# Performance work log

Measured on AMD Instinct MI355X. Metric: run time of the kernel, lower is better.

The kernel has to match this reference:

```python
import jax, jax.numpy as jnp
import numpy as np

B, S, H, L, V, T = 128, 512, 512, 2, 30, 64  # batch, enc len, hidden, layers, vocab, decode len


def _p(k, shape):
    return jax.random.normal(k, shape, jnp.float32) * 0.05


def setup_inputs() -> dict:
    key = jax.random.key(0)
    ks = jax.random.split(key, 24)
    inp = {"x": jax.random.normal(ks[0], (B, S, 2), jnp.float32)}
    inp["emb"] = _p(ks[1], (V, H))
    # encoder GRU (input dim 2 for layer 0, H for layer 1); PyTorch gate order r,z,n
    inp["enc_Wih0"] = _p(ks[2], (3 * H, 2));  inp["enc_Whh0"] = _p(ks[3], (3 * H, H))
    inp["enc_bih0"] = _p(ks[4], (3 * H,));    inp["enc_bhh0"] = _p(ks[5], (3 * H,))
    inp["enc_Wih1"] = _p(ks[6], (3 * H, H));  inp["enc_Whh1"] = _p(ks[7], (3 * H, H))
    inp["enc_bih1"] = _p(ks[8], (3 * H,));    inp["enc_bhh1"] = _p(ks[9], (3 * H,))
    # decoder GRU (input dim H)
    inp["dec_Wih0"] = _p(ks[10], (3 * H, H)); inp["dec_Whh0"] = _p(ks[11], (3 * H, H))
    inp["dec_bih0"] = _p(ks[12], (3 * H,));   inp["dec_bhh0"] = _p(ks[13], (3 * H,))
    inp["dec_Wih1"] = _p(ks[14], (3 * H, H)); inp["dec_Whh1"] = _p(ks[15], (3 * H, H))
    inp["dec_bih1"] = _p(ks[16], (3 * H,));   inp["dec_bhh1"] = _p(ks[17], (3 * H,))
    inp["fc_W"] = _p(ks[18], (V, 2 * H));     inp["fc_b"] = _p(ks[19], (V,))
    return inp


def gru_cell(xt, h, Wih, Whh, bih, bhh):
    gi = xt @ Wih.T + bih
    gh = h @ Whh.T + bhh
    i_r, i_z, i_n = jnp.split(gi, 3, axis=-1)
    h_r, h_z, h_n = jnp.split(gh, 3, axis=-1)
    r = jax.nn.sigmoid(i_r + h_r)
    z = jax.nn.sigmoid(i_z + h_z)
    n = jnp.tanh(i_n + r * h_n)
    return (1.0 - z) * n + z * h


def _forward(x, emb,
             enc_Wih0, enc_Whh0, enc_bih0, enc_bhh0,
             enc_Wih1, enc_Whh1, enc_bih1, enc_bhh1,
             dec_Wih0, dec_Whh0, dec_bih0, dec_bhh0,
             dec_Wih1, dec_Whh1, dec_bih1, dec_bhh1,
             fc_W, fc_b):
    b = x.shape[0]
    h0 = jnp.zeros((b, H), x.dtype)

    # ---- encoder: 2-layer GRU scanned over time ----
    def enc_step(hs, xt):
        a = gru_cell(xt, hs[0], enc_Wih0, enc_Whh0, enc_bih0, enc_bhh0)
        c = gru_cell(a, hs[1], enc_Wih1, enc_Whh1, enc_bih1, enc_bhh1)
        return (a, c), c

    (e0, e1), out_enc_t = jax.lax.scan(enc_step, (h0, h0), x.transpose(1, 0, 2))
    out_enc = out_enc_t.transpose(1, 0, 2)  # [B, S, H]

    def dec_step(carry, _):
        (d0, d1), tok = carry
        e = emb[tok]  # [B, H]
        n0 = gru_cell(e, d0, dec_Wih0, dec_Whh0, dec_bih0, dec_bhh0)
        n1 = gru_cell(n0, d1, dec_Wih1, dec_Whh1, dec_bih1, dec_bhh1)
        out_dec = n1  # [B, H]
        sim = jnp.einsum('bsh,bh->bs', out_enc, out_dec)  # [B, S]
        # faithful to nn.Softmax() implicit dim on 3-D [B,S,1] tensor -> dim=0 (batch)
        att_w = jax.nn.softmax(sim, axis=0)
        attention = jnp.einsum('bs,bsh->bh', att_w, out_enc)  # [B, H]
        logits = jnp.concatenate([out_dec, attention], axis=-1) @ fc_W.T + fc_b  # [B, V]
        tok_next = jnp.argmax(logits, axis=-1)
        return ((n0, n1), tok_next), logits

    tok0 = jnp.zeros((b,), jnp.int32)
    ((f0, f1), _), logits_t = jax.lax.scan(dec_step, ((e0, e1), tok0), None, length=T)
    vec_out = logits_t.transpose(1, 0, 2)  # [B, T, V]
    hidden = jnp.stack([f0, f1], axis=0)   # [n_layers, B, H]
    return vec_out, hidden


def reference(x, emb,
              enc_Wih0, enc_Whh0, enc_bih0, enc_bhh0,
              enc_Wih1, enc_Whh1, enc_bih1, enc_bhh1,
              dec_Wih0, dec_Whh0, dec_bih0, dec_bhh0,
              dec_Wih1, dec_Whh1, dec_bih1, dec_bhh1,
              fc_W, fc_b):
    return _forward(x, emb,
                    enc_Wih0, enc_Whh0, enc_bih0, enc_bhh0,
                    enc_Wih1, enc_Whh1, enc_bih1, enc_bhh1,
                    dec_Wih0, dec_Whh0, dec_bih0, dec_bhh0,
                    dec_Wih1, dec_Whh1, dec_bih1, dec_bhh1,
                    fc_W, fc_b)
```

## Files before the change

kernel.cpp:

```cpp
#include <hip/hip_runtime.h>
#include <math.h>

typedef short  s16x8 __attribute__((ext_vector_type(8)));
typedef float  f32x4 __attribute__((ext_vector_type(4)));
typedef unsigned short u16;
typedef unsigned long long u64;

#define MFMA16(a, b, c) __builtin_amdgcn_mfma_f32_16x16x32_bf16((a), (b), (c), 0, 0, 0)

#define BB 128
#define SS 512
#define HH 512
#define VV 30
#define TT 64

#define SC_SYS  __HIP_MEMORY_SCOPE_SYSTEM

__device__ __forceinline__ float b2f(u16 v) {
  union { unsigned int u; float f; } c; c.u = ((unsigned int)v) << 16; return c.f;
}
__device__ __forceinline__ u16 f2b(float f) {
  union { float f; unsigned int u; } c; c.f = f;
  unsigned int r = (c.u + 0x7FFFu + ((c.u >> 16) & 1u)) >> 16;
  return (u16)r;
}
__device__ __forceinline__ float sigm(float x) { return 1.f / (1.f + expf(-x)); }
__device__ __forceinline__ s16x8 ldf(const u16* p) { return *(const s16x8*)p; }

__device__ __forceinline__ u64  ld64c(const u64* p)      { return __hip_atomic_load(p, __ATOMIC_RELAXED, SC_SYS); }
__device__ __forceinline__ void st64c(u64* p, u64 v)     { __hip_atomic_store(p, v, __ATOMIC_RELAXED, SC_SYS); }
__device__ __forceinline__ void stf32c(float* p, float v){ __hip_atomic_store(p, v, __ATOMIC_RELAXED, SC_SYS); }
__device__ __forceinline__ float ldf32c(const float* p)  { return __hip_atomic_load(p, __ATOMIC_RELAXED, SC_SYS); }
__device__ __forceinline__ void sti32c(int* p, int v)    { __hip_atomic_store(p, v, __ATOMIC_RELAXED, SC_SYS); }
__device__ __forceinline__ int  ldi32c(const int* p)     { return __hip_atomic_load(p, __ATOMIC_RELAXED, SC_SYS); }
__device__ __forceinline__ void stf32(float* p, float v) { *p = v; }

__device__ unsigned int g_slot[736 * 16];
__device__ float g_smx[SS], g_ssum[SS];

#define S_L0  0
#define S_L1  32
#define S_G0  96
#define S_G1  160
#define S_SIM 224
#define S_SMX 480
#define S_ATT 608

__device__ __forceinline__ void pollslot(int idx, int target) {
  if (target <= 0) return;
  const unsigned int* p = &g_slot[idx * 16];
  unsigned long long t0 = __builtin_amdgcn_s_memrealtime();
  while ((int)__hip_atomic_load(p, __ATOMIC_RELAXED, SC_SYS) < target) {
    __builtin_amdgcn_s_sleep(1);
    if (__builtin_amdgcn_s_memrealtime() - t0 > (1ull << 21)) break;
  }
}
__device__ __forceinline__ void wait_group(int base, int n, int target) {
  if ((int)threadIdx.x < n) pollslot(base + (int)threadIdx.x, target);
  __syncthreads();
}
__device__ __forceinline__ void enc_wait(int p) {
  const int t = threadIdx.x;
  if (t < 32) pollslot(S_L0 + t, p);
  else if (t < 96) pollslot(S_L1 + (t - 32), p - 1);
  __syncthreads();
}
__device__ __forceinline__ void postslot(int idx, int val) {
  __syncthreads();
  if (threadIdx.x == 0)
    __hip_atomic_store(&g_slot[idx * 16], (unsigned int)val, __ATOMIC_RELAXED, SC_SYS);
}

__device__ __forceinline__ s16x8 ldl(const u16* buf, int row, int slot) {
  return *(const s16x8*)&buf[(row << 8) + ((slot ^ (row & 15)) << 3)];
}

__device__ __forceinline__ void stage64(u16* SMb, const u16* SRC, int mbase, int kc) {
  const int t = threadIdx.x;
  const u64* base = (const u64*)SRC;
  u64 v[16];
#pragma unroll
  for (int j = 0; j < 16; ++j) {
    const int g = kc * 8 + (j >> 1);
    const int half = j & 1;
    v[j] = ld64c(base + (size_t)(g * 128 + mbase + half * 32) * 8 + t);
  }
#pragma unroll
  for (int j = 0; j < 16; ++j) {
    const int gl = j >> 1, half = j & 1;
    const int row = half * 32 + (t >> 3);
    const int w = t & 7;
    const int s = ((w & 4) << 2) + 2 * gl + ((w >> 1) & 1);
    *(u64*)&SMb[(row << 8) + ((s ^ (row & 15)) << 3) + ((w & 1) << 2)] = v[j];
  }
}

__device__ __forceinline__ void stage128(u16* SM, const u16* SRC, int kc) {
  const int t = threadIdx.x;
  const u64* base = (const u64*)SRC;
  u64 v[32];
#pragma unroll
  for (int j = 0; j < 32; ++j) {
    const int g = kc * 8 + (j >> 2);
    const int q = j & 3;
    v[j] = ld64c(base + (size_t)(g * 128 + q * 32) * 8 + t);
  }
#pragma unroll
  for (int j = 0; j < 32; ++j) {
    const int gl = j >> 2, q = j & 3;
    const int row = q * 32 + (t >> 3);
    const int w = t & 7;
    const int s = ((w & 4) << 2) + 2 * gl + ((w >> 1) & 1);
    *(u64*)&SM[(row << 8) + ((s ^ (row & 15)) << 3) + ((w & 1) << 2)] = v[j];
  }
}


template <bool GATHER, bool COH_H>
__device__ __forceinline__ void gru_dual_staged(
    int bx, u16* SM,
    const u16* __restrict__ A1s, const int* __restrict__ gather,
    const u16* __restrict__ A2s,
    const u16* __restrict__ Wihs, const u16* __restrict__ Whhs,
    const float* __restrict__ bih, const float* __restrict__ bhh,
    float* __restrict__ hf, u16* __restrict__ hs_new,
    u16* __restrict__ oe, size_t oe_mstride)
{
  const int tid  = threadIdx.x;
  const int wave = tid >> 6, lane = tid & 63;
  const int lrow = lane & 15, lq = lane >> 4;
  const int gidx = bx >> 1;
  const int j0 = gidx * 16;
  const int mbase = (bx & 1) * 64;
  const int lr = wave * 16 + lrow;
  const int m0 = mbase + wave * 16;

  const u16* a1p = nullptr;
  if (GATHER)
    a1p = A1s + (size_t)ldi32c(&gather[m0 + lrow]) * 1024 + lq * 8;

  const u16* bp[6];
#pragma unroll
  for (int t = 0; t < 6; ++t) {
    int g = (t < 3) ? t : t - 3;
    const u16* W = (t < 3) ? Wihs : Whhs;
    bp[t] = W + (size_t)(g * HH + j0 + lrow) * 1024 + lq * 8;
  }

  f32x4 acc[6];
#pragma unroll
  for (int t = 0; t < 6; ++t) acc[t] = (f32x4){0.f, 0.f, 0.f, 0.f};

  for (int kc = 0; kc < 4; ++kc) {
    if (!GATHER) stage64(SM, A1s, mbase, kc);
    stage64(SM + 64 * 256, A2s, mbase, kc);
    __syncthreads();
#pragma unroll
    for (int ki = 0; ki < 4; ++ki) {
      const int sl = ki * 4 + lq;
      s16x8 a1h, a1l;
      if (GATHER) { a1h = ldf(a1p); a1l = ldf(a1p + 512); a1p += 32; }
      else        { a1h = ldl(SM, lr, sl); a1l = ldl(SM, lr, 16 + sl); }
      s16x8 a2h = ldl(SM, 64 + lr, sl), a2l = ldl(SM, 64 + lr, 16 + sl);
#pragma unroll
      for (int t = 0; t < 6; ++t) {
        s16x8 bh = ldf(bp[t]), bl = ldf(bp[t] + 512); bp[t] += 32;
        s16x8 ah = (t < 3) ? a1h : a2h;
        s16x8 al = (t < 3) ? a1l : a2l;
        acc[t] = MFMA16(ah, bh, acc[t]);
        acc[t] = MFMA16(ah, bl, acc[t]);
        acc[t] = MFMA16(al, bh, acc[t]);
      }
    }
    __syncthreads();
  }

  const int c = j0 + lrow;
  const float bir = bih[c], biz = bih[HH + c], bin = bih[2 * HH + c];
  const float bhr = bhh[c], bhz = bhh[HH + c], bhn = bhh[2 * HH + c];
  float hvv[4];
#pragma unroll
  for (int r = 0; r < 4; ++r) {
    int m = mbase + wave * 16 + lq * 4 + r;
    float ir = acc[0][r] + bir, iz = acc[1][r] + biz, inn = acc[2][r] + bin;
    float hr = acc[3][r] + bhr, hz = acc[4][r] + bhz, hn = acc[5][r] + bhn;
    float rr = sigm(ir + hr);
    float zz = sigm(iz + hz);
    float nn = tanhf(inn + rr * hn);
    float hp = COH_H ? ldf32c(&hf[(size_t)m * HH + c]) : hf[(size_t)m * HH + c];
    float hv = (1.f - zz) * nn + zz * hp;
    if (COH_H) stf32c(&hf[(size_t)m * HH + c], hv);
    else       stf32(&hf[(size_t)m * HH + c], hv);
    hvv[r] = hv;
    if (oe) oe[(size_t)m * oe_mstride + c] = f2b(hv);
  }
  __syncthreads();
#pragma unroll
  for (int r = 0; r < 4; ++r) {
    const int ml = wave * 16 + lq * 4 + r;
    u16 hi = f2b(hvv[r]);
    SM[ml * 32 + lrow]      = hi;
    SM[ml * 32 + 16 + lrow] = f2b(hvv[r] - b2f(hi));
  }
  __syncthreads();
  {
    u64* dst = (u64*)hs_new + (size_t)(gidx * 128 + mbase) * 8;
    const u64* src = (const u64*)SM;
    st64c(dst + tid,       src[tid]);
    st64c(dst + 256 + tid, src[256 + tid]);
  }
}

__device__ __forceinline__ void gru_l0_staged(
    int bx, int p, u16* SM,
    const float* __restrict__ x, const float* __restrict__ Wih0,
    const u16* __restrict__ Whh0s,
    const float* __restrict__ bih0, const float* __restrict__ bhh0,
    const u16* __restrict__ As,
    float* __restrict__ af, u16* __restrict__ as_new)
{
  const int tid  = threadIdx.x;
  const int wave = tid >> 6, lane = tid & 63;
  const int lrow = lane & 15, lq = lane >> 4;
  const int j0 = bx * 16;
  const int mw = wave * 32;
  const int r0 = mw + lrow, r1 = mw + 16 + lrow;

  const u16* bp[3];
#pragma unroll
  for (int t = 0; t < 3; ++t)
    bp[t] = Whh0s + (size_t)(t * HH + j0 + lrow) * 1024 + lq * 8;

  f32x4 acc[2][3];
#pragma unroll
  for (int i = 0; i < 2; ++i)
#pragma unroll
    for (int t = 0; t < 3; ++t) acc[i][t] = (f32x4){0.f, 0.f, 0.f, 0.f};

  for (int kc = 0; kc < 4; ++kc) {
    stage128(SM, As, kc);
    __syncthreads();
#pragma unroll
    for (int ki = 0; ki < 4; ++ki) {
      const int sl = ki * 4 + lq;
      s16x8 a0h = ldl(SM, r0, sl), a0l = ldl(SM, r0, 16 + sl);
      s16x8 a1h = ldl(SM, r1, sl), a1l = ldl(SM, r1, 16 + sl);
#pragma unroll
      for (int t = 0; t < 3; ++t) {
        s16x8 bh = ldf(bp[t]), bl = ldf(bp[t] + 512); bp[t] += 32;
        acc[0][t] = MFMA16(a0h, bh, acc[0][t]);
        acc[0][t] = MFMA16(a0h, bl, acc[0][t]);
        acc[0][t] = MFMA16(a0l, bh, acc[0][t]);
        acc[1][t] = MFMA16(a1h, bh, acc[1][t]);
        acc[1][t] = MFMA16(a1h, bl, acc[1][t]);
        acc[1][t] = MFMA16(a1l, bh, acc[1][t]);
      }
    }
    __syncthreads();
  }

  const int c = j0 + lrow;
  const float bir = bih0[c], biz = bih0[HH + c], bin = bih0[2 * HH + c];
  const float bhr = bhh0[c], bhz = bhh0[HH + c], bhn = bhh0[2 * HH + c];
  const float wr0 = Wih0[(size_t)c * 2],            wr1 = Wih0[(size_t)c * 2 + 1];
  const float wz0 = Wih0[(size_t)(HH + c) * 2],     wz1 = Wih0[(size_t)(HH + c) * 2 + 1];
  const float wn0 = Wih0[(size_t)(2 * HH + c) * 2], wn1 = Wih0[(size_t)(2 * HH + c) * 2 + 1];
  float hvv[2][4];
#pragma unroll
  for (int tm = 0; tm < 2; ++tm) {
#pragma unroll
    for (int r = 0; r < 4; ++r) {
      int m = mw + tm * 16 + lq * 4 + r;
      float x0 = x[((size_t)m * SS + p) * 2];
      float x1 = x[((size_t)m * SS + p) * 2 + 1];
      float ir  = bir + x0 * wr0 + x1 * wr1;
      float iz  = biz + x0 * wz0 + x1 * wz1;
      float inn = bin + x0 * wn0 + x1 * wn1;
      float hr = acc[tm][0][r] + bhr, hz = acc[tm][1][r] + bhz, hn = acc[tm][2][r] + bhn;
      float rr = sigm(ir + hr);
      float zz = sigm(iz + hz);
      float nn = tanhf(inn + rr * hn);
      float hp = af[(size_t)m * HH + c];
      float hv = (1.f - zz) * nn + zz * hp;
      af[(size_t)m * HH + c] = hv;
      hvv[tm][r] = hv;
    }
  }
  __syncthreads();
#pragma unroll
  for (int tm = 0; tm < 2; ++tm) {
#pragma unroll
    for (int r = 0; r < 4; ++r) {
      const int ml = mw + tm * 16 + lq * 4 + r;
      u16 hi = f2b(hvv[tm][r]);
      SM[ml * 32 + lrow]      = hi;
      SM[ml * 32 + 16 + lrow] = f2b(hvv[tm][r] - b2f(hi));
    }
  }
  __syncthreads();
  {
    u64* dst = (u64*)as_new + (size_t)(bx * 128) * 8;
    const u64* src = (const u64*)SM;
#pragma unroll
    for (int k = 0; k < 4; ++k)
      st64c(dst + k * 256 + tid, src[k * 256 + tid]);
  }
}

__device__ __forceinline__ void sim_block(
    int bx, const float* __restrict__ n1f, const u16* __restrict__ oe,
    float* __restrict__ simt)
{
  const int b = bx >> 1, sc = bx & 1;
  const int wave = threadIdx.x >> 6, lane = threadIdx.x & 63;
  float xr[8];
  const u64* xp = (const u64*)(n1f + (size_t)b * HH + lane * 8);
#pragma unroll
  for (int j = 0; j < 4; ++j) {
    union { u64 q; float f[2]; } u; u.q = ld64c(xp + j);
    xr[2 * j] = u.f[0]; xr[2 * j + 1] = u.f[1];
  }
  int s0 = sc * 256 + wave * 64;
  for (int i = 0; i < 64; ++i) {
    int s = s0 + i;
    s16x8 ov = *(const s16x8*)(oe + ((size_t)b * SS + s) * HH + lane * 8);
    float acc = 0.f;
#pragma unroll
    for (int j = 0; j < 8; ++j) acc += xr[j] * b2f((u16)ov[j]);
    for (int off = 32; off; off >>= 1) acc += __shfl_down(acc, off);
    if (lane == 0) stf32c(&simt[(size_t)s * BB + b], acc);
  }
}

__device__ __forceinline__ void smax_block(int bx, const float* __restrict__ simt)
{
  const int wave = threadIdx.x >> 6, lane = threadIdx.x & 63;
  const int s = bx * 4 + wave;
  union { u64 q; float f[2]; } u;
  u.q = ld64c((const u64*)&simt[(size_t)s * BB + lane * 2]);
  float mx = fmaxf(u.f[0], u.f[1]);
  for (int off = 32; off; off >>= 1) mx = fmaxf(mx, __shfl_xor(mx, off));
  float e = expf(u.f[0] - mx) + expf(u.f[1] - mx);
  for (int off = 32; off; off >>= 1) e += __shfl_xor(e, off);
  if (lane == 0) { stf32c(&g_smx[s], mx); stf32c(&g_ssum[s], e); }
}

__device__ __forceinline__ void attn_block(
    int b, int tstep, const float* __restrict__ simt, const float* __restrict__ n1f,
    const u16* __restrict__ oe, const float* __restrict__ fcW,
    const float* __restrict__ fcb, float* __restrict__ dout,
    int* __restrict__ tok)
{
  __shared__ float wsm[SS];
  __shared__ float xv[2 * HH];
  __shared__ float lg[32];
  const int t = threadIdx.x;

  for (int s = t; s < SS; s += 256) {
    float sv = ldf32c(&simt[(size_t)s * BB + b]);
    float mx = ldf32c(&g_smx[s]);
    float sm = ldf32c(&g_ssum[s]);
    wsm[s] = expf(sv - mx) / sm;
  }
  xv[t]       = ldf32c(&n1f[(size_t)b * HH + t]);
  xv[t + 256] = ldf32c(&n1f[(size_t)b * HH + t + 256]);
  __syncthreads();

  {
    float a0 = 0.f, a1 = 0.f;
    const u16* base = oe + (size_t)b * SS * HH;
    for (int s = 0; s < SS; ++s) {
      float w = wsm[s];
      a0 += w * b2f(base[(size_t)s * HH + t]);
      a1 += w * b2f(base[(size_t)s * HH + t + 256]);
    }
    xv[HH + t]       = a0;
    xv[HH + t + 256] = a1;
  }
  __syncthreads();

  int wave = t >> 6, lane = t & 63;
  for (int v = wave; v < VV; v += 4) {
    const float* wr = fcW + (size_t)v * (2 * HH);
    float acc = 0.f;
#pragma unroll
    for (int i = 0; i < 16; ++i) acc += xv[i * 64 + lane] * wr[i * 64 + lane];
    for (int off = 32; off; off >>= 1) acc += __shfl_down(acc, off);
    if (lane == 0) {
      float lv = acc + fcb[v];
      lg[v] = lv;
      dout[(size_t)b * (TT * VV) + (size_t)tstep * VV + v] = lv;
    }
  }
  __syncthreads();

  if (t == 0) {
    float best = lg[0]; int bi = 0;
    for (int v = 1; v < VV; ++v) if (lg[v] > best) { best = lg[v]; bi = v; }
    sti32c(&tok[b], bi);
  }
}

__global__ __launch_bounds__(256) void enc_persist(
    const float* __restrict__ x, const float* __restrict__ Wih0,
    const u16* __restrict__ Whh0s,
    const float* __restrict__ bih0, const float* __restrict__ bhh0,
    const u16* __restrict__ Wih1s, const u16* __restrict__ Whh1s,
    const float* __restrict__ bih1, const float* __restrict__ bhh1,
    u16* ABF0, u16* ABF1, float* af,
    u16* CBF0, u16* CBF1, float* cf,
    u16* out_enc)
{
  __shared__ u16 SM[32768];
  const int bx = blockIdx.x;
  const u16* pa = ABF0; u16* pa_n = ABF1;
  const u16* pc = CBF0; u16* pc_n = CBF1;
  for (int p = 0; p <= SS; ++p) {
    enc_wait(p);
    if (bx < 32) {
      if (p < SS) {
        gru_l0_staged(bx, p, SM, x, Wih0, Whh0s, bih0, bhh0, pa, af, pa_n);
        postslot(S_L0 + bx, p + 1);
      }
    } else {
      if (p > 0) {
        u16* oe = out_enc + (size_t)(p - 1) * HH;
        gru_dual_staged<false, false>(bx - 32, SM, pa, nullptr, pc,
                                      Wih1s, Whh1s, bih1, bhh1,
                                      cf, pc_n, oe, (size_t)SS * HH);
        postslot(S_L1 + (bx - 32), p);
      }
    }
    const u16* tp;
    tp = pa; pa = pa_n; pa_n = (u16*)tp;
    tp = pc; pc = pc_n; pc_n = (u16*)tp;
  }
}

__global__ __launch_bounds__(256) void dec_persist(
    const u16* __restrict__ EMBs, int* tok,
    const u16* __restrict__ WdIH0, const u16* __restrict__ WdHH0,
    const float* __restrict__ dbih0, const float* __restrict__ dbhh0,
    const u16* __restrict__ WdIH1, const u16* __restrict__ WdHH1,
    const float* __restrict__ dbih1, const float* __restrict__ dbhh1,
    float* af, float* cf,
    u16* D0A, u16* D0B, u16* D1A, u16* D1B,
    const u16* __restrict__ oe, float* simt,
    const float* __restrict__ fcW, const float* __restrict__ fcb,
    float* dout)
{
  __shared__ u16 SM[32768];
  const int bx = blockIdx.x;
  const u16* d0c = D0A; u16* d0n = D0B;
  const u16* d1c = D1A; u16* d1n = D1B;
  for (int t = 0; t < TT; ++t) {
    if (bx < 64) {
      wait_group(S_ATT, 128, t);
      gru_dual_staged<true, false>(bx, SM, EMBs, tok, d0c,
                                   WdIH0, WdHH0, dbih0, dbhh0, af, d0n,
                                   nullptr, 0);
      postslot(S_G0 + bx, t + 1);
    }
    { const u16* tp = d0c; d0c = d0n; d0n = (u16*)tp; }

    if (bx < 64) {
      wait_group(S_G0, 64, t + 1);
      gru_dual_staged<false, true>(bx, SM, d0c, nullptr, d1c,
                                   WdIH1, WdHH1, dbih1, dbhh1, cf, d1n,
                                   nullptr, 0);
      postslot(S_G1 + bx, t + 1);
    }
    { const u16* tp = d1c; d1c = d1n; d1n = (u16*)tp; }

    wait_group(S_G1, 64, t + 1);
    sim_block(bx, cf, oe, simt);
    postslot(S_SIM + bx, t + 1);

    if (bx < 128) {
      wait_group(S_SIM, 256, t + 1);
      smax_block(bx, simt);
      postslot(S_SMX + bx, t + 1);
    }

    if (bx < BB) {
      wait_group(S_SMX, 128, t + 1);
      attn_block(bx, t, simt, cf, oe, fcW, fcb, dout, tok);
      postslot(S_ATT + bx, t + 1);
    }
  }
}

__global__ __launch_bounds__(256) void splitall(
    const float* __restrict__ s0, u16* d0, const float* __restrict__ s1, u16* d1,
    const float* __restrict__ s2, u16* d2, const float* __restrict__ s3, u16* d3,
    const float* __restrict__ s4, u16* d4, const float* __restrict__ s5, u16* d5,
    const float* __restrict__ s6, u16* d6, const float* __restrict__ s7, u16* d7)
{
  const int WN = 3 * HH * HH;
  int i = blockIdx.x * 256 + threadIdx.x;
  const float* s; u16* d; int j;
  if      (i < 1 * WN) { s = s0; d = d0; j = i; }
  else if (i < 2 * WN) { s = s1; d = d1; j = i - 1 * WN; }
  else if (i < 3 * WN) { s = s2; d = d2; j = i - 2 * WN; }
  else if (i < 4 * WN) { s = s3; d = d3; j = i - 3 * WN; }
  else if (i < 5 * WN) { s = s4; d = d4; j = i - 4 * WN; }
  else if (i < 6 * WN) { s = s5; d = d5; j = i - 5 * WN; }
  else if (i < 7 * WN) { s = s6; d = d6; j = i - 6 * WN; }
  else { j = i - 7 * WN; if (j >= VV * HH) return; s = s7; d = d7; }
  int r = j >> 9, k = j & 511;
  float v = s[j];
  u16 hi = f2b(v);
  d[(size_t)r * 1024 + k]       = hi;
  d[(size_t)r * 1024 + 512 + k] = f2b(v - b2f(hi));
}

__global__ __launch_bounds__(256) void initk(
    float* af, float* cf, u16* b0, u16* b1, u16* b2, u16* b3, int* tok)
{
  int i = blockIdx.x * 256 + threadIdx.x;
  b0[i] = 0; b1[i] = 0; b2[i] = 0; b3[i] = 0;
  if (i < BB * HH) { af[i] = 0.f; cf[i] = 0.f; }
  if (i < BB) tok[i] = 0;
  if (i < 736) g_slot[i * 16] = 0;
}

__global__ __launch_bounds__(256) void finalize(
    const float* __restrict__ d0, const float* __restrict__ d1,
    float* __restrict__ oh)
{
  int i = blockIdx.x * 256 + threadIdx.x;
  oh[i]           = d0[i];
  oh[BB * HH + i] = d1[i];
}

extern "C" void kernel_launch(void* const* d_in, const int* in_sizes, int n_in,
                              void* d_out, int out_size, void* d_ws, size_t ws_size,
                              hipStream_t stream) {
  const float* x     = (const float*)d_in[0];
  const float* emb   = (const float*)d_in[1];
  const float* eWih0 = (const float*)d_in[2];
  const float* eWhh0 = (const float*)d_in[3];
  const float* ebih0 = (const float*)d_in[4];
  const float* ebhh0 = (const float*)d_in[5];
  const float* eWih1 = (const float*)d_in[6];
  const float* eWhh1 = (const float*)d_in[7];
  const float* ebih1 = (const float*)d_in[8];
  const float* ebhh1 = (const float*)d_in[9];
  const float* dWih0 = (const float*)d_in[10];
  const float* dWhh0 = (const float*)d_in[11];
  const float* dbih0 = (const float*)d_in[12];
  const float* dbhh0 = (const float*)d_in[13];
  const float* dWih1 = (const float*)d_in[14];
  const float* dWhh1 = (const float*)d_in[15];
  const float* dbih1 = (const float*)d_in[16];
  const float* dbhh1 = (const float*)d_in[17];
  const float* fcW   = (const float*)d_in[18];
  const float* fcb   = (const float*)d_in[19];
  float* dout = (float*)d_out;

  char* wsb = (char*)d_ws;
  float* af   = (float*)(wsb + 0);
  float* cf   = (float*)(wsb + 262144);
  u16* ABF0   = (u16*)(wsb + 524288);
  u16* ABF1   = (u16*)(wsb + 786432);
  u16* CBF0   = (u16*)(wsb + 1048576);
  u16* CBF1   = (u16*)(wsb + 1310720);
  int* tok    = (int*)(wsb + 1572864);
  float* simt = (float*)(wsb + 1573376);
  u16* WeHH0  = (u16*)(wsb + 1835520);
  u16* WeIH1  = (u16*)(wsb + 4981248);
  u16* WeHH1  = (u16*)(wsb + 8126976);
  u16* WdIH0  = (u16*)(wsb + 11272704);
  u16* WdHH0  = (u16*)(wsb + 14418432);
  u16* WdIH1  = (u16*)(wsb + 17564160);
  u16* WdHH1  = (u16*)(wsb + 20709888);
  u16* EMBs   = (u16*)(wsb + 23855616);
  u16* oe     = (u16*)(wsb + 23917056);

  initk<<<512, 256, 0, stream>>>(af, cf, ABF0, ABF1, CBF0, CBF1, tok);

  splitall<<<21564, 256, 0, stream>>>(eWhh0, WeHH0, eWih1, WeIH1, eWhh1, WeHH1,
                                      dWih0, WdIH0, dWhh0, WdHH0, dWih1, WdIH1,
                                      dWhh1, WdHH1, emb, EMBs);

  enc_persist<<<96, 256, 0, stream>>>(x, eWih0, WeHH0, ebih0, ebhh0,
                                      WeIH1, WeHH1, ebih1, ebhh1,
                                      ABF0, ABF1, af, CBF0, CBF1, cf, oe);

  dec_persist<<<256, 256, 0, stream>>>(EMBs, tok, WdIH0, WdHH0, dbih0, dbhh0,
                                       WdIH1, WdHH1, dbih1, dbhh1,
                                       af, cf, ABF0, ABF1, CBF1, CBF0,
                                       oe, simt, fcW, fcb, dout);

  finalize<<<256, 256, 0, stream>>>(af, cf, dout + (size_t)BB * TT * VV);
}
```

Baseline: 24.02 ms.

## Split attention context across all blocks and use finer-grained encoder waits

The decoder's attention-weighted sum over 512 encoder positions moves out of the 128 attention blocks into a new phase that runs on all 256 blocks. Each block handles half the sequence for one batch row, and the two halves are added in attn_block. The encoder's coarse whole-grid wait at the top of each step is replaced by per-k-chunk polling of only the slots each block needs, plus a late wait on layer-1 slots before hidden writes. This adds an extra barrier phase per decode step and reuses the WeHH0 workspace region for patt after the encoder finishes, which costs some synchronization overhead in exchange for more parallelism and better overlap.

```diff
diff --git a/kernel.cpp b/kernel.cpp
--- a/kernel.cpp
+++ b/kernel.cpp
@@ -35,7 +35,7 @@
 __device__ __forceinline__ int  ldi32c(const int* p)     { return __hip_atomic_load(p, __ATOMIC_RELAXED, SC_SYS); }
 __device__ __forceinline__ void stf32(float* p, float v) { *p = v; }
 
-__device__ unsigned int g_slot[736 * 16];
+__device__ unsigned int g_slot[992 * 16];
 __device__ float g_smx[SS], g_ssum[SS];
 
 #define S_L0  0
@@ -45,6 +45,7 @@
 #define S_SIM 224
 #define S_SMX 480
 #define S_ATT 608
+#define S_PAT 736
 
 __device__ __forceinline__ void pollslot(int idx, int target) {
   if (target <= 0) return;
@@ -59,12 +60,6 @@
   if ((int)threadIdx.x < n) pollslot(base + (int)threadIdx.x, target);
   __syncthreads();
 }
-__device__ __forceinline__ void enc_wait(int p) {
-  const int t = threadIdx.x;
-  if (t < 32) pollslot(S_L0 + t, p);
-  else if (t < 96) pollslot(S_L1 + (t - 32), p - 1);
-  __syncthreads();
-}
 __device__ __forceinline__ void postslot(int idx, int val) {
   __syncthreads();
   if (threadIdx.x == 0)
@@ -116,9 +111,9 @@
 }
 
 
-template <bool GATHER, bool COH_H>
+template <bool GATHER, bool COH_H, bool EWAIT>
 __device__ __forceinline__ void gru_dual_staged(
-    int bx, u16* SM,
+    int bx, int p, u16* SM,
     const u16* __restrict__ A1s, const int* __restrict__ gather,
     const u16* __restrict__ A2s,
     const u16* __restrict__ Wihs, const u16* __restrict__ Whhs,
@@ -152,6 +147,11 @@
   for (int t = 0; t < 6; ++t) acc[t] = (f32x4){0.f, 0.f, 0.f, 0.f};
 
   for (int kc = 0; kc < 4; ++kc) {
+    if (EWAIT) {
+      if (tid < 8)       pollslot(S_L0 + 8 * kc + tid, p);
+      else if (tid < 16) pollslot(S_L1 + 2 * (8 * kc + (tid - 8)) + (bx & 1), p - 1);
+      __syncthreads();
+    }
     if (!GATHER) stage64(SM, A1s, mbase, kc);
     stage64(SM + 64 * 256, A2s, mbase, kc);
     __syncthreads();
@@ -238,6 +238,8 @@
     for (int t = 0; t < 3; ++t) acc[i][t] = (f32x4){0.f, 0.f, 0.f, 0.f};
 
   for (int kc = 0; kc < 4; ++kc) {
+    if (tid < 8) pollslot(S_L0 + 8 * kc + tid, p);
+    __syncthreads();
     stage128(SM, As, kc);
     __syncthreads();
 #pragma unroll
@@ -286,6 +288,7 @@
       hvv[tm][r] = hv;
     }
   }
+  if (tid < 64) pollslot(S_L1 + tid, p - 1);
   __syncthreads();
 #pragma unroll
   for (int tm = 0; tm < 2; ++tm) {
@@ -345,38 +348,44 @@
   if (lane == 0) { stf32c(&g_smx[s], mx); stf32c(&g_ssum[s], e); }
 }
 
+__device__ __forceinline__ void pat_block(
+    int bx, const float* __restrict__ simt, const u16* __restrict__ oe,
+    float* __restrict__ patt)
+{
+  __shared__ float pw[256];
+  const int b = bx >> 1, sc = bx & 1;
+  const int t = threadIdx.x;
+  const int s = sc * 256 + t;
+  float sv = ldf32c(&simt[(size_t)s * BB + b]);
+  pw[t] = expf(sv - ldf32c(&g_smx[s])) / ldf32c(&g_ssum[s]);
+  __syncthreads();
+  const u16* base = oe + ((size_t)b * SS + sc * 256) * HH;
+  float a0 = 0.f, a1 = 0.f;
+  for (int i = 0; i < 256; ++i) {
+    float w = pw[i];
+    unsigned int v = *(const unsigned int*)&base[(size_t)i * HH + 2 * t];
+    a0 += w * b2f((u16)(v & 0xffffu));
+    a1 += w * b2f((u16)(v >> 16));
+  }
+  stf32c(&patt[((size_t)b * 2 + sc) * HH + 2 * t],     a0);
+  stf32c(&patt[((size_t)b * 2 + sc) * HH + 2 * t + 1], a1);
+}
+
 __device__ __forceinline__ void attn_block(
-    int b, int tstep, const float* __restrict__ simt, const float* __restrict__ n1f,
-    const u16* __restrict__ oe, const float* __restrict__ fcW,
-    const float* __restrict__ fcb, float* __restrict__ dout,
-    int* __restrict__ tok)
-{
-  __shared__ float wsm[SS];
+    int b, int tstep, const float* __restrict__ patt, const float* __restrict__ n1f,
+    const float* __restrict__ fcW, const float* __restrict__ fcb,
+    float* __restrict__ dout, int* __restrict__ tok)
+{
   __shared__ float xv[2 * HH];
   __shared__ float lg[32];
   const int t = threadIdx.x;
 
-  for (int s = t; s < SS; s += 256) {
-    float sv = ldf32c(&simt[(size_t)s * BB + b]);
-    float mx = ldf32c(&g_smx[s]);
-    float sm = ldf32c(&g_ssum[s]);
-    wsm[s] = expf(sv - mx) / sm;
-  }
   xv[t]       = ldf32c(&n1f[(size_t)b * HH + t]);
   xv[t + 256] = ldf32c(&n1f[(size_t)b * HH + t + 256]);
-  __syncthreads();
-
-  {
-    float a0 = 0.f, a1 = 0.f;
-    const u16* base = oe + (size_t)b * SS * HH;
-    for (int s = 0; s < SS; ++s) {
-      float w = wsm[s];
-      a0 += w * b2f(base[(size_t)s * HH + t]);
-      a1 += w * b2f(base[(size_t)s * HH + t + 256]);
-    }
-    xv[HH + t]       = a0;
-    xv[HH + t + 256] = a1;
-  }
+  xv[HH + t]       = ldf32c(&patt[(size_t)(b * 2) * HH + t])
+                   + ldf32c(&patt[(size_t)(b * 2 + 1) * HH + t]);
+  xv[HH + t + 256] = ldf32c(&patt[(size_t)(b * 2) * HH + t + 256])
+                   + ldf32c(&patt[(size_t)(b * 2 + 1) * HH + t + 256]);
   __syncthreads();
 
   int wave = t >> 6, lane = t & 63;
@@ -416,7 +425,6 @@
   const u16* pa = ABF0; u16* pa_n = ABF1;
   const u16* pc = CBF0; u16* pc_n = CBF1;
   for (int p = 0; p <= SS; ++p) {
-    enc_wait(p);
     if (bx < 32) {
       if (p < SS) {
         gru_l0_staged(bx, p, SM, x, Wih0, Whh0s, bih0, bhh0, pa, af, pa_n);
@@ -425,9 +433,9 @@
     } else {
       if (p > 0) {
         u16* oe = out_enc + (size_t)(p - 1) * HH;
-        gru_dual_staged<false, false>(bx - 32, SM, pa, nullptr, pc,
-                                      Wih1s, Whh1s, bih1, bhh1,
-                                      cf, pc_n, oe, (size_t)SS * HH);
+        gru_dual_staged<false, false, true>(bx - 32, p, SM, pa, nullptr, pc,
+                                            Wih1s, Whh1s, bih1, bhh1,
+                                            cf, pc_n, oe, (size_t)SS * HH);
         postslot(S_L1 + (bx - 32), p);
       }
     }
@@ -445,7 +453,7 @@
     const float* __restrict__ dbih1, const float* __restrict__ dbhh1,
     float* af, float* cf,
     u16* D0A, u16* D0B, u16* D1A, u16* D1B,
-    const u16* __restrict__ oe, float* simt,
+    const u16* __restrict__ oe, float* simt, float* patt,
     const float* __restrict__ fcW, const float* __restrict__ fcb,
     float* dout)
 {
@@ -456,18 +464,18 @@
   for (int t = 0; t < TT; ++t) {
     if (bx < 64) {
       wait_group(S_ATT, 128, t);
-      gru_dual_staged<true, false>(bx, SM, EMBs, tok, d0c,
-                                   WdIH0, WdHH0, dbih0, dbhh0, af, d0n,
-                                   nullptr, 0);
+      gru_dual_staged<true, false, false>(bx, 0, SM, EMBs, tok, d0c,
+                                          WdIH0, WdHH0, dbih0, dbhh0, af, d0n,
+                                          nullptr, 0);
       postslot(S_G0 + bx, t + 1);
     }
     { const u16* tp = d0c; d0c = d0n; d0n = (u16*)tp; }
 
     if (bx < 64) {
       wait_group(S_G0, 64, t + 1);
-      gru_dual_staged<false, true>(bx, SM, d0c, nullptr, d1c,
-                                   WdIH1, WdHH1, dbih1, dbhh1, cf, d1n,
-                                   nullptr, 0);
+      gru_dual_staged<false, true, false>(bx, 0, SM, d0c, nullptr, d1c,
+                                          WdIH1, WdHH1, dbih1, dbhh1, cf, d1n,
+                                          nullptr, 0);
       postslot(S_G1 + bx, t + 1);
     }
     { const u16* tp = d1c; d1c = d1n; d1n = (u16*)tp; }
@@ -482,9 +490,13 @@
       postslot(S_SMX + bx, t + 1);
     }
 
+    wait_group(S_SMX, 128, t + 1);
+    pat_block(bx, simt, oe, patt);
+    postslot(S_PAT + bx, t + 1);
+
     if (bx < BB) {
-      wait_group(S_SMX, 128, t + 1);
-      attn_block(bx, t, simt, cf, oe, fcW, fcb, dout, tok);
+      wait_group(S_PAT, 256, t + 1);
+      attn_block(bx, t, patt, cf, fcW, fcb, dout, tok);
       postslot(S_ATT + bx, t + 1);
     }
   }
@@ -521,7 +533,7 @@
   b0[i] = 0; b1[i] = 0; b2[i] = 0; b3[i] = 0;
   if (i < BB * HH) { af[i] = 0.f; cf[i] = 0.f; }
   if (i < BB) tok[i] = 0;
-  if (i < 736) g_slot[i * 16] = 0;
+  if (i < 992) g_slot[i * 16] = 0;
 }
 
 __global__ __launch_bounds__(256) void finalize(
@@ -576,6 +588,7 @@
   u16* WdHH1  = (u16*)(wsb + 20709888);
   u16* EMBs   = (u16*)(wsb + 23855616);
   u16* oe     = (u16*)(wsb + 23917056);
+  float* patt = (float*)(wsb + 1835520);
 
   initk<<<512, 256, 0, stream>>>(af, cf, ABF0, ABF1, CBF0, CBF1, tok);
 
@@ -590,7 +603,7 @@
   dec_persist<<<256, 256, 0, stream>>>(EMBs, tok, WdIH0, WdHH0, dbih0, dbhh0,
                                        WdIH1, WdHH1, dbih1, dbhh1,
                                        af, cf, ABF0, ABF1, CBF1, CBF0,
-                                       oe, simt, fcW, fcb, dout);
+                                       oe, simt, patt, fcW, fcb, dout);
 
   finalize<<<256, 256, 0, stream>>>(af, cf, dout + (size_t)BB * TT * VV);
 }
```

Result: no change. 24.22 ms (+0.9%).

## Refine encoder waits to per-chunk slots and fuse softmax stats into attention

Applied to the files above, without the earlier changes.

Encoder blocks no longer wait for every dependency at the start of a step. Each k-chunk now polls only the producer slots it needs just before staging that chunk, so compute can begin earlier and overlap with late producers. The decoder's separate softmax-statistics phase, along with its grid-wide wait, is removed: each attention block recomputes the per-position max and sum over the batch itself, trading redundant reads and exp calls for one fewer global synchronisation per step. The polling loop also checks the timeout clock only every 32 iterations.

```diff
diff --git a/kernel.cpp b/kernel.cpp
--- a/kernel.cpp
+++ b/kernel.cpp
@@ -35,34 +35,28 @@
 __device__ __forceinline__ int  ldi32c(const int* p)     { return __hip_atomic_load(p, __ATOMIC_RELAXED, SC_SYS); }
 __device__ __forceinline__ void stf32(float* p, float v) { *p = v; }
 
-__device__ unsigned int g_slot[736 * 16];
-__device__ float g_smx[SS], g_ssum[SS];
+__device__ unsigned int g_slot[992 * 16];
 
 #define S_L0  0
 #define S_L1  32
 #define S_G0  96
 #define S_G1  160
 #define S_SIM 224
-#define S_SMX 480
 #define S_ATT 608
 
 __device__ __forceinline__ void pollslot(int idx, int target) {
   if (target <= 0) return;
   const unsigned int* p = &g_slot[idx * 16];
   unsigned long long t0 = __builtin_amdgcn_s_memrealtime();
+  int c = 0;
   while ((int)__hip_atomic_load(p, __ATOMIC_RELAXED, SC_SYS) < target) {
     __builtin_amdgcn_s_sleep(1);
-    if (__builtin_amdgcn_s_memrealtime() - t0 > (1ull << 21)) break;
+    if (((++c) & 31) == 0 &&
+        __builtin_amdgcn_s_memrealtime() - t0 > (1ull << 21)) break;
   }
 }
 __device__ __forceinline__ void wait_group(int base, int n, int target) {
   if ((int)threadIdx.x < n) pollslot(base + (int)threadIdx.x, target);
-  __syncthreads();
-}
-__device__ __forceinline__ void enc_wait(int p) {
-  const int t = threadIdx.x;
-  if (t < 32) pollslot(S_L0 + t, p);
-  else if (t < 96) pollslot(S_L1 + (t - 32), p - 1);
   __syncthreads();
 }
 __device__ __forceinline__ void postslot(int idx, int val) {
@@ -116,9 +110,9 @@
 }
 
 
-template <bool GATHER, bool COH_H>
+template <bool GATHER, bool COH_H, bool EWAIT>
 __device__ __forceinline__ void gru_dual_staged(
-    int bx, u16* SM,
+    int bx, int p, u16* SM,
     const u16* __restrict__ A1s, const int* __restrict__ gather,
     const u16* __restrict__ A2s,
     const u16* __restrict__ Wihs, const u16* __restrict__ Whhs,
@@ -152,6 +146,11 @@
   for (int t = 0; t < 6; ++t) acc[t] = (f32x4){0.f, 0.f, 0.f, 0.f};
 
   for (int kc = 0; kc < 4; ++kc) {
+    if (EWAIT) {
+      if (tid < 8)       pollslot(S_L0 + 8 * kc + tid, p);
+      else if (tid < 16) pollslot(S_L1 + 2 * (8 * kc + (tid - 8)) + (bx & 1), p - 1);
+      __syncthreads();
+    }
     if (!GATHER) stage64(SM, A1s, mbase, kc);
     stage64(SM + 64 * 256, A2s, mbase, kc);
     __syncthreads();
@@ -238,6 +237,8 @@
     for (int t = 0; t < 3; ++t) acc[i][t] = (f32x4){0.f, 0.f, 0.f, 0.f};
 
   for (int kc = 0; kc < 4; ++kc) {
+    if (tid < 8) pollslot(S_L0 + 8 * kc + tid, p);
+    __syncthreads();
     stage128(SM, As, kc);
     __syncthreads();
 #pragma unroll
@@ -286,6 +287,7 @@
       hvv[tm][r] = hv;
     }
   }
+  if (tid < 64) pollslot(S_L1 + tid, p - 1);
   __syncthreads();
 #pragma unroll
   for (int tm = 0; tm < 2; ++tm) {
@@ -332,19 +334,6 @@
   }
 }
 
-__device__ __forceinline__ void smax_block(int bx, const float* __restrict__ simt)
-{
-  const int wave = threadIdx.x >> 6, lane = threadIdx.x & 63;
-  const int s = bx * 4 + wave;
-  union { u64 q; float f[2]; } u;
-  u.q = ld64c((const u64*)&simt[(size_t)s * BB + lane * 2]);
-  float mx = fmaxf(u.f[0], u.f[1]);
-  for (int off = 32; off; off >>= 1) mx = fmaxf(mx, __shfl_xor(mx, off));
-  float e = expf(u.f[0] - mx) + expf(u.f[1] - mx);
-  for (int off = 32; off; off >>= 1) e += __shfl_xor(e, off);
-  if (lane == 0) { stf32c(&g_smx[s], mx); stf32c(&g_ssum[s], e); }
-}
-
 __device__ __forceinline__ void attn_block(
     int b, int tstep, const float* __restrict__ simt, const float* __restrict__ n1f,
     const u16* __restrict__ oe, const float* __restrict__ fcW,
@@ -357,10 +346,19 @@
   const int t = threadIdx.x;
 
   for (int s = t; s < SS; s += 256) {
-    float sv = ldf32c(&simt[(size_t)s * BB + b]);
-    float mx = ldf32c(&g_smx[s]);
-    float sm = ldf32c(&g_ssum[s]);
-    wsm[s] = expf(sv - mx) / sm;
+    const u64* rp = (const u64*)(simt + (size_t)s * BB);
+    float mx = -1e30f;
+    for (int i = 0; i < 64; ++i) {
+      union { u64 q; float f[2]; } u; u.q = ld64c(rp + i);
+      mx = fmaxf(mx, fmaxf(u.f[0], u.f[1]));
+    }
+    float e = 0.f, sv = 0.f;
+    for (int i = 0; i < 64; ++i) {
+      union { u64 q; float f[2]; } u; u.q = ld64c(rp + i);
+      e += expf(u.f[0] - mx) + expf(u.f[1] - mx);
+      if (i == (b >> 1)) sv = (b & 1) ? u.f[1] : u.f[0];
+    }
+    wsm[s] = expf(sv - mx) / e;
   }
   xv[t]       = ldf32c(&n1f[(size_t)b * HH + t]);
   xv[t + 256] = ldf32c(&n1f[(size_t)b * HH + t + 256]);
@@ -416,7 +414,6 @@
   const u16* pa = ABF0; u16* pa_n = ABF1;
   const u16* pc = CBF0; u16* pc_n = CBF1;
   for (int p = 0; p <= SS; ++p) {
-    enc_wait(p);
     if (bx < 32) {
       if (p < SS) {
         gru_l0_staged(bx, p, SM, x, Wih0, Whh0s, bih0, bhh0, pa, af, pa_n);
@@ -425,9 +422,9 @@
     } else {
       if (p > 0) {
         u16* oe = out_enc + (size_t)(p - 1) * HH;
-        gru_dual_staged<false, false>(bx - 32, SM, pa, nullptr, pc,
-                                      Wih1s, Whh1s, bih1, bhh1,
-                                      cf, pc_n, oe, (size_t)SS * HH);
+        gru_dual_staged<false, false, true>(bx - 32, p, SM, pa, nullptr, pc,
+                                            Wih1s, Whh1s, bih1, bhh1,
+                                            cf, pc_n, oe, (size_t)SS * HH);
         postslot(S_L1 + (bx - 32), p);
       }
     }
@@ -456,18 +453,18 @@
   for (int t = 0; t < TT; ++t) {
     if (bx < 64) {
       wait_group(S_ATT, 128, t);
-      gru_dual_staged<true, false>(bx, SM, EMBs, tok, d0c,
-                                   WdIH0, WdHH0, dbih0, dbhh0, af, d0n,
-                                   nullptr, 0);
+      gru_dual_staged<true, false, false>(bx, 0, SM, EMBs, tok, d0c,
+                                          WdIH0, WdHH0, dbih0, dbhh0, af, d0n,
+                                          nullptr, 0);
       postslot(S_G0 + bx, t + 1);
     }
     { const u16* tp = d0c; d0c = d0n; d0n = (u16*)tp; }
 
     if (bx < 64) {
       wait_group(S_G0, 64, t + 1);
-      gru_dual_staged<false, true>(bx, SM, d0c, nullptr, d1c,
-                                   WdIH1, WdHH1, dbih1, dbhh1, cf, d1n,
-                                   nullptr, 0);
+      gru_dual_staged<false, true, false>(bx, 0, SM, d0c, nullptr, d1c,
+                                          WdIH1, WdHH1, dbih1, dbhh1, cf, d1n,
+                                          nullptr, 0);
       postslot(S_G1 + bx, t + 1);
     }
     { const u16* tp = d1c; d1c = d1n; d1n = (u16*)tp; }
@@ -476,14 +473,8 @@
     sim_block(bx, cf, oe, simt);
     postslot(S_SIM + bx, t + 1);
 
-    if (bx < 128) {
+    if (bx < BB) {
       wait_group(S_SIM, 256, t + 1);
-      smax_block(bx, simt);
-      postslot(S_SMX + bx, t + 1);
-    }
-
-    if (bx < BB) {
-      wait_group(S_SMX, 128, t + 1);
       attn_block(bx, t, simt, cf, oe, fcW, fcb, dout, tok);
       postslot(S_ATT + bx, t + 1);
     }
@@ -521,7 +512,7 @@
   b0[i] = 0; b1[i] = 0; b2[i] = 0; b3[i] = 0;
   if (i < BB * HH) { af[i] = 0.f; cf[i] = 0.f; }
   if (i < BB) tok[i] = 0;
-  if (i < 736) g_slot[i * 16] = 0;
+  if (i < 992) g_slot[i * 16] = 0;
 }
 
 __global__ __launch_bounds__(256) void finalize(
```

New measurement: 27.13 ms. +13.0%, slower.
